# Performance work log

Measured on AMD Instinct MI355X. Metric: run time of the kernel, lower is better.

Reference implementation:

```python
import jax, jax.numpy as jnp
import numpy as np


def setup_inputs() -> dict:
    key = jax.random.key(0)
    ks = jax.random.split(key, 8)
    B, S, K, D = 2, 64, 64, 256
    C = D // 8
    return {
        "x": jax.random.normal(ks[0], (B, S, K, D), dtype=jnp.float32),
        "Wq": jax.random.normal(ks[1], (C, D), dtype=jnp.float32) * (1.0 / np.sqrt(D)),
        "bq": jax.random.normal(ks[2], (C,), dtype=jnp.float32) * 0.01,
        "Wk": jax.random.normal(ks[3], (C, D), dtype=jnp.float32) * (1.0 / np.sqrt(D)),
        "bk": jax.random.normal(ks[4], (C,), dtype=jnp.float32) * 0.01,
        "Wv": jax.random.normal(ks[5], (D, D), dtype=jnp.float32) * (1.0 / np.sqrt(D)),
        "bv": jax.random.normal(ks[6], (D,), dtype=jnp.float32) * 0.01,
        "gamma": jax.random.uniform(ks[7], (1,), dtype=jnp.float32),
    }


def reference(x, Wq, bq, Wk, bk, Wv, bv, gamma):
    # x: [B, S, K, D]
    B, S, K, D = x.shape
    N = K * S
    # torch: x.permute(0,3,2,1) -> [B, D, K, S]; flatten (K,S) -> N (n = k*S + s)
    xp = jnp.transpose(x, (0, 3, 2, 1)).reshape(B, D, N)  # [B, D, N]
    # 1x1 convs == per-token linear maps over the channel dim
    q = jnp.einsum('cd,bdn->bnc', Wq, xp) + bq            # [B, N, C]
    k = jnp.einsum('cd,bdn->bcn', Wk, xp) + bk[:, None]   # [B, C, N]
    energy = jnp.einsum('bnc,bcm->bnm', q, k)             # [B, N, N]
    attention = jax.nn.softmax(energy, axis=-1)           # rows sum to 1
    v = jnp.einsum('ed,bdn->ben', Wv, xp) + bv[:, None]   # [B, D, N]
    # out[b,d,i] = sum_j V[b,d,j] * A[b,i,j]
    out = jnp.einsum('bdj,bij->bdi', v, attention)        # [B, D, N]
    out = gamma * out + xp                                # residual with learned scale
    out = out.reshape(B, D, K, S)
    return jnp.transpose(out, (0, 3, 2, 1))               # [B, S, K, D]
```

## Files before the change

### kernel.cpp

```cpp
#include <hip/hip_runtime.h>
#include <stdint.h>
#include <math.h>

using short8   = __attribute__((ext_vector_type(8))) short;
using ushort4v = __attribute__((ext_vector_type(4))) unsigned short;
using f32x4    = __attribute__((ext_vector_type(4))) float;
using uint4v   = __attribute__((ext_vector_type(4))) unsigned int;

#define B_ 2
#define S_ 64
#define K_ 64
#define D_ 256
#define C_ 32
#define N_ 4096
#define LOG2E 1.4426950408889634f

__device__ __forceinline__ float b2f(unsigned short u) {
    unsigned int v = ((unsigned int)u) << 16;
    return __builtin_bit_cast(float, v);
}
__device__ __forceinline__ unsigned short f2b(float f) {
    unsigned int x = __builtin_bit_cast(unsigned int, f);
    x += 0x7fffu + ((x >> 16) & 1u);
    return (unsigned short)(x >> 16);
}
__device__ __forceinline__ unsigned int pk2(float a, float b) {
    unsigned int xa = __builtin_bit_cast(unsigned int, a);
    unsigned int xb = __builtin_bit_cast(unsigned int, b);
    xa += 0x7fffu + ((xa >> 16) & 1u);
    xb += 0x7fffu + ((xb >> 16) & 1u);
    return (xa >> 16) | (xb & 0xffff0000u);
}

__global__ __launch_bounds__(256) void wcvt_kernel(
    const float* __restrict__ Wq, const float* __restrict__ bq,
    const float* __restrict__ Wk, const float* __restrict__ bk,
    const float* __restrict__ Wv, const float* __restrict__ bv,
    unsigned short* __restrict__ Wh, unsigned short* __restrict__ Wl,
    float* __restrict__ bcat)
{
    int oc = blockIdx.x;
    int d  = threadIdx.x;
    float w;
    if (oc < 32)       w = Wq[oc * 256 + d] * LOG2E;
    else if (oc < 64)  w = Wk[(oc - 32) * 256 + d];
    else               w = Wv[(oc - 64) * 256 + d];
    unsigned short h = f2b(w);
    Wh[oc * 256 + d] = h;
    Wl[oc * 256 + d] = f2b(w - b2f(h));
    if (d == 0) {
        float bb;
        if (oc < 32)      bb = bq[oc] * LOG2E;
        else if (oc < 64) bb = bk[oc - 32];
        else              bb = bv[oc - 64];
        bcat[oc] = bb;
    }
}

__global__ __launch_bounds__(256) void qkv_kernel(
    const float* __restrict__ x,
    const unsigned short* __restrict__ Wh, const unsigned short* __restrict__ Wl,
    const float* __restrict__ bcat,
    unsigned short* __restrict__ Qh, unsigned short* __restrict__ Ql,
    unsigned short* __restrict__ Kh, unsigned short* __restrict__ Kl,
    unsigned short* __restrict__ Vm)
{
    __shared__ unsigned short lxh[16 * 256];
    __shared__ unsigned short lxl[16 * 256];

    int tid = threadIdx.x;
    int bid = blockIdx.x;
    int b  = bid >> 8;
    int n0 = (bid & 255) << 4;

    {
        int tt = tid >> 4, dg0 = (tid & 15) * 16;
        int n = n0 + tt;
        int s = n & 63, kk = n >> 6;
        const float* xr = x + (((size_t)(b * S_ + s)) * K_ + kk) * D_ + dg0;
        short8 h0, l0, h1, l1;
#pragma unroll
        for (int e = 0; e < 8; ++e) {
            float v = xr[e];
            unsigned short hh = f2b(v);
            h0[e] = (short)hh; l0[e] = (short)f2b(v - b2f(hh));
        }
#pragma unroll
        for (int e = 0; e < 8; ++e) {
            float v = xr[8 + e];
            unsigned short hh = f2b(v);
            h1[e] = (short)hh; l1[e] = (short)f2b(v - b2f(hh));
        }
        int m0 = dg0 >> 3;
        int sw0 = ((m0 ^ (tt & 7)) << 3);
        int sw1 = (((m0 + 1) ^ (tt & 7)) << 3);
        *(short8*)(lxh + tt * 256 + sw0) = h0;
        *(short8*)(lxh + tt * 256 + sw1) = h1;
        *(short8*)(lxl + tt * 256 + sw0) = l0;
        *(short8*)(lxl + tt * 256 + sw1) = l1;
    }
    __syncthreads();

    int wave = tid >> 6, lane = tid & 63;
    int col = lane & 15, g = lane >> 4;

#pragma unroll
    for (int i = 0; i < 5; ++i) {
        int ct = wave + i * 4;
        int oc0 = ct * 16;
        const unsigned short* whr = Wh + (size_t)(oc0 + col) * 256;
        const unsigned short* wlr = Wl + (size_t)(oc0 + col) * 256;
        f32x4 acc = {0.f, 0.f, 0.f, 0.f};

        if (ct < 4) {
#pragma unroll
            for (int dc = 0; dc < 8; ++dc) {
                int sw = (((dc * 4 + g) ^ (col & 7)) << 3);
                short8 xh8 = *(const short8*)(lxh + col * 256 + sw);
                short8 xl8 = *(const short8*)(lxl + col * 256 + sw);
                short8 wh8 = *(const short8*)(whr + dc * 32 + g * 8);
                short8 wl8 = *(const short8*)(wlr + dc * 32 + g * 8);
                acc = __builtin_amdgcn_mfma_f32_16x16x32_bf16(xl8, wh8, acc, 0, 0, 0);
                acc = __builtin_amdgcn_mfma_f32_16x16x32_bf16(xh8, wl8, acc, 0, 0, 0);
                acc = __builtin_amdgcn_mfma_f32_16x16x32_bf16(xh8, wh8, acc, 0, 0, 0);
            }
            float bb = bcat[oc0 + col];
            unsigned short* Th = (ct < 2) ? Qh : Kh;
            unsigned short* Tl = (ct < 2) ? Ql : Kl;
            int c0 = (ct & 1) * 16;
#pragma unroll
            for (int r = 0; r < 4; ++r) {
                int tok = n0 + g * 4 + r;
                float v = acc[r] + bb;
                unsigned short hh = f2b(v);
                size_t idx = ((size_t)b * N_ + tok) * C_ + c0 + col;
                Th[idx] = hh;
                Tl[idx] = f2b(v - b2f(hh));
            }
        } else {
#pragma unroll
            for (int dc = 0; dc < 8; ++dc) {
                int sw = (((dc * 4 + g) ^ (col & 7)) << 3);
                short8 xh8 = *(const short8*)(lxh + col * 256 + sw);
                short8 wh8 = *(const short8*)(whr + dc * 32 + g * 8);
                acc = __builtin_amdgcn_mfma_f32_16x16x32_bf16(xh8, wh8, acc, 0, 0, 0);
            }
            float bb = bcat[oc0 + col];
            int c0 = oc0 - 64;
            ushort4v st;
#pragma unroll
            for (int r = 0; r < 4; ++r) st[r] = f2b(acc[r] + bb);
            int tok0 = n0 + g * 4;
            int s0 = 8 * g + ((n0 & 16) >> 2);
            int d_ch = c0 + col;
            int o = d_ch * 64 + s0 * 2;
            o ^= (d_ch & 7) << 4;
            size_t vbyteoff = ((size_t)b * (N_ / 32) + (tok0 >> 5)) * (D_ * 32 * 2)
                            + (size_t)o;
            *(ushort4v*)((char*)Vm + vbyteoff) = st;
        }
    }
}

__global__ __launch_bounds__(512, 2) void attn_kernel(
    const unsigned short* __restrict__ Qh, const unsigned short* __restrict__ Ql,
    const unsigned short* __restrict__ Kh, const unsigned short* __restrict__ Kl,
    const unsigned short* __restrict__ Vm,
    float* __restrict__ O_part, float* __restrict__ lsum_part)
{
    __shared__ __align__(16) char vlds[2][16384];
    __shared__ __align__(16) char plds[2 * 8192];

    int tid  = threadIdx.x;
    int wave = tid >> 6;
    int lane = tid & 63;
    int col = lane & 15, g = lane >> 4;
    int qq = wave >> 1;
    int dh = wave & 1;
    int dbase = dh * 128;
    int tid16 = tid * 16;
    int lane16 = lane * 16;

    int bid = blockIdx.x;
    int x7 = bid & 7;
    int b  = x7 >> 2;
    int ks = x7 & 3;
    int qt = bid >> 3;
    int q0 = qt * 128 + qq * 32;
    int jbase = ks * (N_ / 4);

    size_t qoff = ((size_t)b * N_ + q0 + dh * 16 + col) * C_ + g * 8;
    short8 qfh = *(const short8*)(Qh + qoff);
    short8 qfl = *(const short8*)(Ql + qoff);

    f32x4 acc[2][8];
#pragma unroll
    for (int qs = 0; qs < 2; ++qs)
#pragma unroll
        for (int dt = 0; dt < 8; ++dt) acc[qs][dt] = (f32x4){0.f, 0.f, 0.f, 0.f};
    float l_run = 0.f;

    const unsigned short* kbh = Kh + (size_t)b * N_ * C_;
    const unsigned short* kbl = Kl + (size_t)b * N_ * C_;
    const char* vbyte = (const char*)Vm + (size_t)b * ((size_t)N_ * D_ * 2);

    auto kaddr0 = [&](int it) { return (size_t)(jbase + it * 32 + col) * C_ + g * 8; };
    auto kaddr1 = [&](int it) { return (size_t)(jbase + it * 32 + 16 + col) * C_ + g * 8; };

    unsigned vro = (unsigned)(((dbase + col) * 64 + g * 16) ^ ((col & 7) << 4));
    char* pmy = plds + qq * 2048 + dh * 1024 + lane16;
    const char* pr0 = plds + qq * 2048 + lane16;
    const char* pr1 = plds + qq * 2048 + 1024 + lane16;

    {
        const char* vsrc = vbyte + (size_t)(ks * 32) * 16384 + tid16;
        f32x4 s0 = *(const f32x4*)(vsrc);
        f32x4 s1 = *(const f32x4*)(vsrc + 8192);
        *(f32x4*)(vlds[0] + tid16)        = s0;
        *(f32x4*)(vlds[0] + tid16 + 8192) = s1;
    }
    short8 kh0A = *(const short8*)(kbh + kaddr0(0));
    short8 kl0A = *(const short8*)(kbl + kaddr0(0));
    short8 kh1A = *(const short8*)(kbh + kaddr1(0));
    short8 kl1A = *(const short8*)(kbl + kaddr1(0));
    short8 kh0B = *(const short8*)(kbh + kaddr0(1));
    short8 kl0B = *(const short8*)(kbl + kaddr0(1));
    short8 kh1B = *(const short8*)(kbh + kaddr1(1));
    short8 kl1B = *(const short8*)(kbl + kaddr1(1));
    {
        f32x4 z = {0.f, 0.f, 0.f, 0.f};
        f32x4 sa = __builtin_amdgcn_mfma_f32_16x16x32_bf16(kl0A, qfh, z, 0, 0, 0);
        sa = __builtin_amdgcn_mfma_f32_16x16x32_bf16(kh0A, qfl, sa, 0, 0, 0);
        sa = __builtin_amdgcn_mfma_f32_16x16x32_bf16(kh0A, qfh, sa, 0, 0, 0);
        f32x4 sb = __builtin_amdgcn_mfma_f32_16x16x32_bf16(kl1A, qfh, z, 0, 0, 0);
        sb = __builtin_amdgcn_mfma_f32_16x16x32_bf16(kh1A, qfl, sb, 0, 0, 0);
        sb = __builtin_amdgcn_mfma_f32_16x16x32_bf16(kh1A, qfh, sb, 0, 0, 0);
        float pa[4], pb[4];
#pragma unroll
        for (int r = 0; r < 4; ++r) { pa[r] = exp2f(sa[r]); pb[r] = exp2f(sb[r]); }
        l_run += (pa[0] + pa[1]) + (pa[2] + pa[3]) + (pb[0] + pb[1]) + (pb[2] + pb[3]);
        uint4v uo;
        uo[0] = pk2(pa[0], pa[1]); uo[1] = pk2(pa[2], pa[3]);
        uo[2] = pk2(pb[0], pb[1]); uo[3] = pk2(pb[2], pb[3]);
        *(uint4v*)(pmy) = uo;
    }
    __syncthreads();

#define ATTN_PHASE(IT, CKH0, CKL0, CKH1, CKL1, NKH0, NKL0, NKH1, NKL1)           \
    {                                                                            \
        int itn_ = (IT) + 1;                                                     \
        int itk_ = (IT) + 2;         \
        const char* vsrc_ = vbyte + (size_t)(ks * 32 + itn_) * 16384 + tid16;    \
        f32x4 stg0_ = *(const f32x4*)(vsrc_);                                    \
        f32x4 stg1_ = *(const f32x4*)(vsrc_ + 8192);                             \
        NKH0 = *(const short8*)(kbh + kaddr0(itk_));                             \
        NKL0 = *(const short8*)(kbl + kaddr0(itk_));                             \
        NKH1 = *(const short8*)(kbh + kaddr1(itk_));                             \
        NKL1 = *(const short8*)(kbl + kaddr1(itk_));                             \
        __builtin_amdgcn_sched_barrier(0);        \
        f32x4 z_ = {0.f, 0.f, 0.f, 0.f};                                         \
        f32x4 sa_ = __builtin_amdgcn_mfma_f32_16x16x32_bf16(CKL0, qfh, z_, 0, 0, 0); \
        sa_ = __builtin_amdgcn_mfma_f32_16x16x32_bf16(CKH0, qfl, sa_, 0, 0, 0);  \
        sa_ = __builtin_amdgcn_mfma_f32_16x16x32_bf16(CKH0, qfh, sa_, 0, 0, 0);  \
        f32x4 sb_ = __builtin_amdgcn_mfma_f32_16x16x32_bf16(CKL1, qfh, z_, 0, 0, 0); \
        sb_ = __builtin_amdgcn_mfma_f32_16x16x32_bf16(CKH1, qfl, sb_, 0, 0, 0);  \
        sb_ = __builtin_amdgcn_mfma_f32_16x16x32_bf16(CKH1, qfh, sb_, 0, 0, 0);  \
        float pa_[4], pb_[4];                                                    \
        _Pragma("unroll")                                                        \
        for (int r = 0; r < 4; ++r) { pa_[r] = exp2f(sa_[r]); pb_[r] = exp2f(sb_[r]); } \
        l_run += (pa_[0] + pa_[1]) + (pa_[2] + pa_[3])                           \
               + (pb_[0] + pb_[1]) + (pb_[2] + pb_[3]);                          \
        uint4v uo_;                                                              \
        uo_[0] = pk2(pa_[0], pa_[1]); uo_[1] = pk2(pa_[2], pa_[3]);              \
        uo_[2] = pk2(pb_[0], pb_[1]); uo_[3] = pk2(pb_[2], pb_[3]);              \
        int rb_ = (IT) & 1, wb_ = (itn_) & 1;                                    \
        short8 pf0_ = *(const short8*)(pr0 + rb_ * 8192);                        \
        short8 pf1_ = *(const short8*)(pr1 + rb_ * 8192);                        \
        short8 vf_[8];                                                           \
        _Pragma("unroll")                                                        \
        for (int dt = 0; dt < 8; ++dt)                                           \
            vf_[dt] = *(const short8*)(vlds[rb_] + vro + dt * 1024);             \
        _Pragma("unroll")                                                        \
        for (int dt = 0; dt < 8; ++dt) {                                         \
            acc[0][dt] = __builtin_amdgcn_mfma_f32_16x16x32_bf16(vf_[dt], pf0_, acc[0][dt], 0, 0, 0); \
            acc[1][dt] = __builtin_amdgcn_mfma_f32_16x16x32_bf16(vf_[dt], pf1_, acc[1][dt], 0, 0, 0); \
        }                                                                        \
        *(uint4v*)(pmy + wb_ * 8192) = uo_;                                      \
        *(f32x4*)(vlds[wb_] + tid16)        = stg0_;                             \
        *(f32x4*)(vlds[wb_] + tid16 + 8192) = stg1_;                             \
        __syncthreads();                                                         \
    }

    for (int it2 = 0; it2 < 15; ++it2) {
        int itA = it2 * 2, itB = itA + 1;
        ATTN_PHASE(itA, kh0B, kl0B, kh1B, kl1B, kh0A, kl0A, kh1A, kl1A);
        ATTN_PHASE(itB, kh0A, kl0A, kh1A, kl1A, kh0B, kl0B, kh1B, kl1B);
    }
    ATTN_PHASE(30, kh0B, kl0B, kh1B, kl1B, kh0A, kl0A, kh1A, kl1A);
#undef ATTN_PHASE

    {
        short8 pf0 = *(const short8*)(pr0 + 8192);
        short8 pf1 = *(const short8*)(pr1 + 8192);
        short8 vf[8];
#pragma unroll
        for (int dt = 0; dt < 8; ++dt)
            vf[dt] = *(const short8*)(vlds[1] + vro + dt * 1024);
#pragma unroll
        for (int dt = 0; dt < 8; ++dt) {
            acc[0][dt] = __builtin_amdgcn_mfma_f32_16x16x32_bf16(vf[dt], pf0, acc[0][dt], 0, 0, 0);
            acc[1][dt] = __builtin_amdgcn_mfma_f32_16x16x32_bf16(vf[dt], pf1, acc[1][dt], 0, 0, 0);
        }
    }

    l_run += __shfl_xor(l_run, 16); l_run += __shfl_xor(l_run, 32);

    float* op = O_part + (size_t)bid * 32768 + wave * 4096;
#pragma unroll
    for (int qs = 0; qs < 2; ++qs)
#pragma unroll
        for (int dt = 0; dt < 8; ++dt) {
            int j = qs * 8 + dt;
            *(f32x4*)(op + j * 256 + col * 16 + g * 4) = acc[qs][dt];
        }
    if (g == 0)
        lsum_part[bid * 128 + qq * 32 + dh * 16 + col] = l_run;
}

__global__ __launch_bounds__(256) void epi_kernel(
    const float* __restrict__ O_part, const float* __restrict__ lsum_part,
    const float* __restrict__ x, const float* __restrict__ gamma_p,
    float* __restrict__ out)
{
    int gid = blockIdx.x * 256 + threadIdx.x;
    int d  = (gid & 63) * 4;
    int nl = gid >> 6;
    int b  = nl >> 12;
    int n  = nl & (N_ - 1);

    int qt = n >> 7, qq = (n >> 5) & 3, qs = (n >> 4) & 1, col = n & 15;
    int dh = d >> 7, dt = (d >> 4) & 7;
    int w = qq * 2 + dh, j = qs * 8 + dt;
    int boff = w * 4096 + j * 256 + col * 16 + (d & 15);
    int loff = qq * 32 + qs * 16 + col;

    f32x4 acc = {0.f, 0.f, 0.f, 0.f};
    float l = 0.f;
#pragma unroll
    for (int ks = 0; ks < 4; ++ks) {
        int bid = qt * 8 + b * 4 + ks;
        f32x4 p = *(const f32x4*)(O_part + (size_t)bid * 32768 + boff);
        acc[0] += p[0]; acc[1] += p[1]; acc[2] += p[2]; acc[3] += p[3];
        l += lsum_part[bid * 128 + loff];
    }
    float scale = gamma_p[0] / l;
    int s = n & 63, kk = n >> 6;
    size_t o = (((size_t)(b * S_ + s)) * K_ + kk) * D_ + d;
    f32x4 xv = *(const f32x4*)(x + o);
    f32x4 ov;
#pragma unroll
    for (int e = 0; e < 4; ++e) ov[e] = acc[e] * scale + xv[e];
    *(f32x4*)(out + o) = ov;
}

extern "C" void kernel_launch(void* const* d_in, const int* in_sizes, int n_in,
                              void* d_out, int out_size, void* d_ws, size_t ws_size,
                              hipStream_t stream) {
    const float* x  = (const float*)d_in[0];
    const float* Wq = (const float*)d_in[1];
    const float* bq = (const float*)d_in[2];
    const float* Wk = (const float*)d_in[3];
    const float* bk = (const float*)d_in[4];
    const float* Wv = (const float*)d_in[5];
    const float* bv = (const float*)d_in[6];
    const float* gm = (const float*)d_in[7];

    char* ws = (char*)d_ws;
    unsigned short* Wh   = (unsigned short*)(ws);
    unsigned short* Wl   = (unsigned short*)(ws + 0x40000);
    float*          bcat = (float*)         (ws + 0x80000);
    unsigned short* Qh   = (unsigned short*)(ws + 0x100000);
    unsigned short* Ql   = (unsigned short*)(ws + 0x180000);
    unsigned short* Kh   = (unsigned short*)(ws + 0x200000);
    unsigned short* Kl   = (unsigned short*)(ws + 0x280000);
    unsigned short* Vm   = (unsigned short*)(ws + 0x300000);
    float*          Op   = (float*)         (ws + 0x700000);
    float*          lp   = (float*)         (ws + 0x2700000);
    float* o = (float*)d_out;

    wcvt_kernel<<<320, 256, 0, stream>>>(Wq, bq, Wk, bk, Wv, bv, Wh, Wl, bcat);
    qkv_kernel<<<512, 256, 0, stream>>>(x, Wh, Wl, bcat, Qh, Ql, Kh, Kl, Vm);
    attn_kernel<<<256, 512, 0, stream>>>(Qh, Ql, Kh, Kl, Vm, Op, lp);
    epi_kernel<<<2048, 256, 0, stream>>>(Op, lp, x, gm, o);
}
```

Baseline: 69.44 us.

## Double attention block to 1024 threads, splitting key halves and D quarters per wave

Each attention block now runs 16 waves instead of 8. Each wave computes QK^T for a single 16-key half and one query subtile, and accumulates PV over a quarter of D. The goal is to cut per-wave register pressure and serial work and to raise latency hiding, so the per-block LDS staging is split across more threads. The row-sum partials are now stored per key half and combined in the epilogue. The cost is more waves contending for barriers and LDS, and a launch_bounds of (1024,4) that may be unachievable and so cap registers.

```diff
diff --git a/kernel.cpp b/kernel.cpp
--- a/kernel.cpp
+++ b/kernel.cpp
@@ -6,6 +6,7 @@
 using ushort4v = __attribute__((ext_vector_type(4))) unsigned short;
 using f32x4    = __attribute__((ext_vector_type(4))) float;
 using uint4v   = __attribute__((ext_vector_type(4))) unsigned int;
+using uint2v   = __attribute__((ext_vector_type(2))) unsigned int;
 
 #define B_ 2
 #define S_ 64
@@ -162,7 +163,7 @@
     }
 }
 
-__global__ __launch_bounds__(512, 2) void attn_kernel(
+__global__ __launch_bounds__(1024, 4) void attn_kernel(
     const unsigned short* __restrict__ Qh, const unsigned short* __restrict__ Ql,
     const unsigned short* __restrict__ Kh, const unsigned short* __restrict__ Kl,
     const unsigned short* __restrict__ Vm,
@@ -175,9 +176,10 @@
     int wave = tid >> 6;
     int lane = tid & 63;
     int col = lane & 15, g = lane >> 4;
-    int qq = wave >> 1;
-    int dh = wave & 1;
-    int dbase = dh * 128;
+    int qq = wave >> 2;
+    int dq = wave & 3;
+    int kh = dq & 1;
+    int qs_own = dq >> 1;
     int tid16 = tid * 16;
     int lane16 = lane * 16;
 
@@ -189,125 +191,107 @@
     int q0 = qt * 128 + qq * 32;
     int jbase = ks * (N_ / 4);
 
-    size_t qoff = ((size_t)b * N_ + q0 + dh * 16 + col) * C_ + g * 8;
+    size_t qoff = ((size_t)b * N_ + q0 + qs_own * 16 + col) * C_ + g * 8;
     short8 qfh = *(const short8*)(Qh + qoff);
     short8 qfl = *(const short8*)(Ql + qoff);
 
-    f32x4 acc[2][8];
+    f32x4 acc[2][4];
 #pragma unroll
     for (int qs = 0; qs < 2; ++qs)
 #pragma unroll
-        for (int dt = 0; dt < 8; ++dt) acc[qs][dt] = (f32x4){0.f, 0.f, 0.f, 0.f};
+        for (int dt = 0; dt < 4; ++dt) acc[qs][dt] = (f32x4){0.f, 0.f, 0.f, 0.f};
     float l_run = 0.f;
 
     const unsigned short* kbh = Kh + (size_t)b * N_ * C_;
     const unsigned short* kbl = Kl + (size_t)b * N_ * C_;
     const char* vbyte = (const char*)Vm + (size_t)b * ((size_t)N_ * D_ * 2);
 
-    auto kaddr0 = [&](int it) { return (size_t)(jbase + it * 32 + col) * C_ + g * 8; };
-    auto kaddr1 = [&](int it) { return (size_t)(jbase + it * 32 + 16 + col) * C_ + g * 8; };
-
-    unsigned vro = (unsigned)(((dbase + col) * 64 + g * 16) ^ ((col & 7) << 4));
-    char* pmy = plds + qq * 2048 + dh * 1024 + lane16;
-    const char* pr0 = plds + qq * 2048 + lane16;
-    const char* pr1 = plds + qq * 2048 + 1024 + lane16;
+    auto kaddr = [&](int it) {
+        return (size_t)(jbase + it * 32 + kh * 16 + col) * C_ + g * 8;
+    };
+
+    unsigned vro = (unsigned)(((dq * 64 + col) * 64 + g * 16) ^ ((col & 7) << 4));
+    int st = qq * 2 + qs_own;
+    char* pmy = plds + st * 1024 + lane16 + kh * 8;
+    const char* pr0 = plds + (qq * 2) * 1024 + lane16;
+    const char* pr1 = plds + (qq * 2 + 1) * 1024 + lane16;
 
     {
         const char* vsrc = vbyte + (size_t)(ks * 32) * 16384 + tid16;
-        f32x4 s0 = *(const f32x4*)(vsrc);
-        f32x4 s1 = *(const f32x4*)(vsrc + 8192);
-        *(f32x4*)(vlds[0] + tid16)        = s0;
-        *(f32x4*)(vlds[0] + tid16 + 8192) = s1;
-    }
-    short8 kh0A = *(const short8*)(kbh + kaddr0(0));
-    short8 kl0A = *(const short8*)(kbl + kaddr0(0));
-    short8 kh1A = *(const short8*)(kbh + kaddr1(0));
-    short8 kl1A = *(const short8*)(kbl + kaddr1(0));
-    short8 kh0B = *(const short8*)(kbh + kaddr0(1));
-    short8 kl0B = *(const short8*)(kbl + kaddr0(1));
-    short8 kh1B = *(const short8*)(kbh + kaddr1(1));
-    short8 kl1B = *(const short8*)(kbl + kaddr1(1));
+        *(f32x4*)(vlds[0] + tid16) = *(const f32x4*)(vsrc);
+    }
+    short8 khA = *(const short8*)(kbh + kaddr(0));
+    short8 klA = *(const short8*)(kbl + kaddr(0));
+    short8 khB = *(const short8*)(kbh + kaddr(1));
+    short8 klB = *(const short8*)(kbl + kaddr(1));
     {
         f32x4 z = {0.f, 0.f, 0.f, 0.f};
-        f32x4 sa = __builtin_amdgcn_mfma_f32_16x16x32_bf16(kl0A, qfh, z, 0, 0, 0);
-        sa = __builtin_amdgcn_mfma_f32_16x16x32_bf16(kh0A, qfl, sa, 0, 0, 0);
-        sa = __builtin_amdgcn_mfma_f32_16x16x32_bf16(kh0A, qfh, sa, 0, 0, 0);
-        f32x4 sb = __builtin_amdgcn_mfma_f32_16x16x32_bf16(kl1A, qfh, z, 0, 0, 0);
-        sb = __builtin_amdgcn_mfma_f32_16x16x32_bf16(kh1A, qfl, sb, 0, 0, 0);
-        sb = __builtin_amdgcn_mfma_f32_16x16x32_bf16(kh1A, qfh, sb, 0, 0, 0);
-        float pa[4], pb[4];
-#pragma unroll
-        for (int r = 0; r < 4; ++r) { pa[r] = exp2f(sa[r]); pb[r] = exp2f(sb[r]); }
-        l_run += (pa[0] + pa[1]) + (pa[2] + pa[3]) + (pb[0] + pb[1]) + (pb[2] + pb[3]);
-        uint4v uo;
+        f32x4 sa = __builtin_amdgcn_mfma_f32_16x16x32_bf16(klA, qfh, z, 0, 0, 0);
+        sa = __builtin_amdgcn_mfma_f32_16x16x32_bf16(khA, qfl, sa, 0, 0, 0);
+        sa = __builtin_amdgcn_mfma_f32_16x16x32_bf16(khA, qfh, sa, 0, 0, 0);
+        float pa[4];
+#pragma unroll
+        for (int r = 0; r < 4; ++r) pa[r] = exp2f(sa[r]);
+        l_run += (pa[0] + pa[1]) + (pa[2] + pa[3]);
+        uint2v uo;
         uo[0] = pk2(pa[0], pa[1]); uo[1] = pk2(pa[2], pa[3]);
-        uo[2] = pk2(pb[0], pb[1]); uo[3] = pk2(pb[2], pb[3]);
-        *(uint4v*)(pmy) = uo;
+        *(uint2v*)(pmy) = uo;
     }
     __syncthreads();
 
-#define ATTN_PHASE(IT, CKH0, CKL0, CKH1, CKL1, NKH0, NKL0, NKH1, NKL1)           \
+#define ATTN_PHASE(IT, CKH, CKL, NKH, NKL)                                       \
     {                                                                            \
         int itn_ = (IT) + 1;                                                     \
         int itk_ = (IT) + 2;         \
         const char* vsrc_ = vbyte + (size_t)(ks * 32 + itn_) * 16384 + tid16;    \
-        f32x4 stg0_ = *(const f32x4*)(vsrc_);                                    \
-        f32x4 stg1_ = *(const f32x4*)(vsrc_ + 8192);                             \
-        NKH0 = *(const short8*)(kbh + kaddr0(itk_));                             \
-        NKL0 = *(const short8*)(kbl + kaddr0(itk_));                             \
-        NKH1 = *(const short8*)(kbh + kaddr1(itk_));                             \
-        NKL1 = *(const short8*)(kbl + kaddr1(itk_));                             \
+        f32x4 stg_ = *(const f32x4*)(vsrc_);                                     \
+        NKH = *(const short8*)(kbh + kaddr(itk_));                               \
+        NKL = *(const short8*)(kbl + kaddr(itk_));                               \
         __builtin_amdgcn_sched_barrier(0);        \
         f32x4 z_ = {0.f, 0.f, 0.f, 0.f};                                         \
-        f32x4 sa_ = __builtin_amdgcn_mfma_f32_16x16x32_bf16(CKL0, qfh, z_, 0, 0, 0); \
-        sa_ = __builtin_amdgcn_mfma_f32_16x16x32_bf16(CKH0, qfl, sa_, 0, 0, 0);  \
-        sa_ = __builtin_amdgcn_mfma_f32_16x16x32_bf16(CKH0, qfh, sa_, 0, 0, 0);  \
-        f32x4 sb_ = __builtin_amdgcn_mfma_f32_16x16x32_bf16(CKL1, qfh, z_, 0, 0, 0); \
-        sb_ = __builtin_amdgcn_mfma_f32_16x16x32_bf16(CKH1, qfl, sb_, 0, 0, 0);  \
-        sb_ = __builtin_amdgcn_mfma_f32_16x16x32_bf16(CKH1, qfh, sb_, 0, 0, 0);  \
-        float pa_[4], pb_[4];                                                    \
+        f32x4 sa_ = __builtin_amdgcn_mfma_f32_16x16x32_bf16(CKL, qfh, z_, 0, 0, 0); \
+        sa_ = __builtin_amdgcn_mfma_f32_16x16x32_bf16(CKH, qfl, sa_, 0, 0, 0);   \
+        sa_ = __builtin_amdgcn_mfma_f32_16x16x32_bf16(CKH, qfh, sa_, 0, 0, 0);   \
+        float pa_[4];                                                            \
         _Pragma("unroll")                                                        \
-        for (int r = 0; r < 4; ++r) { pa_[r] = exp2f(sa_[r]); pb_[r] = exp2f(sb_[r]); } \
-        l_run += (pa_[0] + pa_[1]) + (pa_[2] + pa_[3])                           \
-               + (pb_[0] + pb_[1]) + (pb_[2] + pb_[3]);                          \
-        uint4v uo_;                                                              \
+        for (int r = 0; r < 4; ++r) pa_[r] = exp2f(sa_[r]);                      \
+        l_run += (pa_[0] + pa_[1]) + (pa_[2] + pa_[3]);                          \
+        uint2v uo_;                                                              \
         uo_[0] = pk2(pa_[0], pa_[1]); uo_[1] = pk2(pa_[2], pa_[3]);              \
-        uo_[2] = pk2(pb_[0], pb_[1]); uo_[3] = pk2(pb_[2], pb_[3]);              \
         int rb_ = (IT) & 1, wb_ = (itn_) & 1;                                    \
         short8 pf0_ = *(const short8*)(pr0 + rb_ * 8192);                        \
         short8 pf1_ = *(const short8*)(pr1 + rb_ * 8192);                        \
-        short8 vf_[8];                                                           \
+        short8 vf_[4];                                                           \
         _Pragma("unroll")                                                        \
-        for (int dt = 0; dt < 8; ++dt)                                           \
+        for (int dt = 0; dt < 4; ++dt)                                           \
             vf_[dt] = *(const short8*)(vlds[rb_] + vro + dt * 1024);             \
         _Pragma("unroll")                                                        \
-        for (int dt = 0; dt < 8; ++dt) {                                         \
+        for (int dt = 0; dt < 4; ++dt) {                                         \
             acc[0][dt] = __builtin_amdgcn_mfma_f32_16x16x32_bf16(vf_[dt], pf0_, acc[0][dt], 0, 0, 0); \
             acc[1][dt] = __builtin_amdgcn_mfma_f32_16x16x32_bf16(vf_[dt], pf1_, acc[1][dt], 0, 0, 0); \
         }                                                                        \
-        *(uint4v*)(pmy + wb_ * 8192) = uo_;                                      \
-        *(f32x4*)(vlds[wb_] + tid16)        = stg0_;                             \
-        *(f32x4*)(vlds[wb_] + tid16 + 8192) = stg1_;                             \
+        *(uint2v*)(pmy + wb_ * 8192) = uo_;                                      \
+        *(f32x4*)(vlds[wb_] + tid16) = stg_;                                     \
         __syncthreads();                                                         \
     }
 
     for (int it2 = 0; it2 < 15; ++it2) {
         int itA = it2 * 2, itB = itA + 1;
-        ATTN_PHASE(itA, kh0B, kl0B, kh1B, kl1B, kh0A, kl0A, kh1A, kl1A);
-        ATTN_PHASE(itB, kh0A, kl0A, kh1A, kl1A, kh0B, kl0B, kh1B, kl1B);
-    }
-    ATTN_PHASE(30, kh0B, kl0B, kh1B, kl1B, kh0A, kl0A, kh1A, kl1A);
+        ATTN_PHASE(itA, khB, klB, khA, klA);
+        ATTN_PHASE(itB, khA, klA, khB, klB);
+    }
+    ATTN_PHASE(30, khB, klB, khA, klA);
 #undef ATTN_PHASE
 
     {
         short8 pf0 = *(const short8*)(pr0 + 8192);
         short8 pf1 = *(const short8*)(pr1 + 8192);
-        short8 vf[8];
-#pragma unroll
-        for (int dt = 0; dt < 8; ++dt)
+        short8 vf[4];
+#pragma unroll
+        for (int dt = 0; dt < 4; ++dt)
             vf[dt] = *(const short8*)(vlds[1] + vro + dt * 1024);
 #pragma unroll
-        for (int dt = 0; dt < 8; ++dt) {
+        for (int dt = 0; dt < 4; ++dt) {
             acc[0][dt] = __builtin_amdgcn_mfma_f32_16x16x32_bf16(vf[dt], pf0, acc[0][dt], 0, 0, 0);
             acc[1][dt] = __builtin_amdgcn_mfma_f32_16x16x32_bf16(vf[dt], pf1, acc[1][dt], 0, 0, 0);
         }
@@ -315,16 +299,16 @@
 
     l_run += __shfl_xor(l_run, 16); l_run += __shfl_xor(l_run, 32);
 
-    float* op = O_part + (size_t)bid * 32768 + wave * 4096;
+    float* op = O_part + (size_t)bid * 32768 + (qq * 2 + (dq >> 1)) * 4096;
 #pragma unroll
     for (int qs = 0; qs < 2; ++qs)
 #pragma unroll
-        for (int dt = 0; dt < 8; ++dt) {
-            int j = qs * 8 + dt;
+        for (int dt = 0; dt < 4; ++dt) {
+            int j = qs * 8 + (dq & 1) * 4 + dt;
             *(f32x4*)(op + j * 256 + col * 16 + g * 4) = acc[qs][dt];
         }
     if (g == 0)
-        lsum_part[bid * 128 + qq * 32 + dh * 16 + col] = l_run;
+        lsum_part[bid * 256 + kh * 128 + qq * 32 + qs_own * 16 + col] = l_run;
 }
 
 __global__ __launch_bounds__(256) void epi_kernel(
@@ -351,7 +335,7 @@
         int bid = qt * 8 + b * 4 + ks;
         f32x4 p = *(const f32x4*)(O_part + (size_t)bid * 32768 + boff);
         acc[0] += p[0]; acc[1] += p[1]; acc[2] += p[2]; acc[3] += p[3];
-        l += lsum_part[bid * 128 + loff];
+        l += lsum_part[bid * 256 + loff] + lsum_part[bid * 256 + 128 + loff];
     }
     float scale = gamma_p[0] / l;
     int s = n & 63, kk = n >> 6;
@@ -390,6 +374,6 @@
 
     wcvt_kernel<<<320, 256, 0, stream>>>(Wq, bq, Wk, bk, Wv, bv, Wh, Wl, bcat);
     qkv_kernel<<<512, 256, 0, stream>>>(x, Wh, Wl, bcat, Qh, Ql, Kh, Kl, Vm);
-    attn_kernel<<<256, 512, 0, stream>>>(Qh, Ql, Kh, Kl, Vm, Op, lp);
+    attn_kernel<<<256, 1024, 0, stream>>>(Qh, Ql, Kh, Kl, Vm, Op, lp);
     epi_kernel<<<2048, 256, 0, stream>>>(Op, lp, x, gm, o);
 }
```

After: 68.41 us. Within noise of the previous version (-1.5%).
